# Performance work log

Hardware: AMD Instinct MI355X
Metric: run time of the kernel (lower is better)

## Reference

```python
import jax, jax.numpy as jnp
import numpy as np

B, E, NV = 2, 400000, 50000
DE, DV, DC, DOUT = 64, 64, 32, 64
DIN = DE + 2 * DV + DC  # 224


def setup_inputs() -> dict:
    key = jax.random.key(0)
    ks = jax.random.split(key, 7)
    edata = jax.random.normal(ks[0], (B, E, DE), dtype=jnp.float32)
    vdata = jax.random.normal(ks[1], (B, NV, DV), dtype=jnp.float32)
    cdata = jax.random.normal(ks[2], (B, DC), dtype=jnp.float32)
    sender_ids = jax.random.randint(ks[3], (B, E), 0, NV, dtype=jnp.int64)
    receiver_ids = jax.random.randint(ks[4], (B, E), 0, NV, dtype=jnp.int64)
    W = jax.random.normal(ks[5], (DIN, DOUT), dtype=jnp.float32) * (1.0 / np.sqrt(DIN))
    b = jnp.zeros((DOUT,), dtype=jnp.float32)
    return {"edata": edata, "vdata": vdata, "cdata": cdata,
            "sender_ids": sender_ids, "receiver_ids": receiver_ids,
            "W": W, "b": b}


def reference(edata, vdata, cdata, sender_ids, receiver_ids, W, b):
    # gather sender/receiver vertex features: [B,E,DV]
    sender_data = jnp.take_along_axis(vdata, sender_ids[..., None], axis=1)
    receiver_data = jnp.take_along_axis(vdata, receiver_ids[..., None], axis=1)
    # broadcast context per edge: [B,E,DC]
    curr_cdata = jnp.broadcast_to(cdata[:, None, :], (cdata.shape[0], edata.shape[1], cdata.shape[1]))
    # concat along feature dim -> [B,E,DIN], then per-edge-type MLP updater
    etin = jnp.concatenate((edata, sender_data, receiver_data, curr_cdata), axis=2)
    etout = jax.nn.relu(jnp.einsum("bei,io->beo", etin, W) + b)
    return etout
```

## Files before the change

### kernel.cpp

```cpp
#include <hip/hip_runtime.h>
#include <hip/hip_bf16.h>

typedef __bf16 bf16x8 __attribute__((ext_vector_type(8)));
typedef float  f32x4  __attribute__((ext_vector_type(4)));

#define DE_   64
#define DV_   64
#define DC_   32
#define DOUT_ 64
#define DIN_  224
#define NFRAG 28

__global__ void prep_w_kernel(const float* __restrict__ W, __bf16* __restrict__ wf) {
    int f    = blockIdx.x;
    int lane = threadIdx.x;
    int ks = f >> 2, nt = f & 3;
    int col = nt * 16 + (lane & 15);
    int k0  = ks * 32 + (lane >> 4) * 8;
    bf16x8 v;
#pragma unroll
    for (int j = 0; j < 8; ++j)
        v[j] = (__bf16)W[(k0 + j) * DOUT_ + col];
    reinterpret_cast<bf16x8*>(wf)[f * 64 + lane] = v;
}

__global__ __launch_bounds__(256, 6)
void edge_mlp_kernel(const float* __restrict__ edata,
                     const float* __restrict__ vdata,
                     const float* __restrict__ cdata,
                     const int*   __restrict__ snd,
                     const int*   __restrict__ rcv,
                     const __bf16* __restrict__ wf,
                     const float* __restrict__ bias,
                     float* __restrict__ out,
                     int NV, int n_tiles, int tiles_per_batch) {
    const int lane = threadIdx.x & 63;
    const int tile = blockIdx.x * (blockDim.x >> 6) + (threadIdx.x >> 6);
    if (tile >= n_tiles) return;

    const int lr = lane & 15;
    const int lg = lane >> 4;
    const int kl = lg * 8;

    const int  b   = (tile >= tiles_per_batch) ? 1 : 0;
    const long row = (long)tile * 16 + lr;
    const int  s   = snd[row];
    const int  r   = rcv[row];
    const float* vb = vdata + (long)b * NV * DV_;

    float4 f0[7], f1[7];
#pragma unroll
    for (int ks = 0; ks < 7; ++ks) {
        const float* p;
        if      (ks < 2) p = edata + row * DE_ + ks * 32 + kl;
        else if (ks < 4) p = vb + (long)s * DV_ + (ks - 2) * 32 + kl;
        else if (ks < 6) p = vb + (long)r * DV_ + (ks - 4) * 32 + kl;
        else             p = cdata + b * DC_ + kl;
        f0[ks] = *reinterpret_cast<const float4*>(p);
        f1[ks] = *reinterpret_cast<const float4*>(p + 4);
    }

    float bias_v[4];
#pragma unroll
    for (int nt = 0; nt < 4; ++nt) bias_v[nt] = bias[nt * 16 + lr];

    f32x4 acc[4];
#pragma unroll
    for (int nt = 0; nt < 4; ++nt) acc[nt] = f32x4{0.f, 0.f, 0.f, 0.f};

#pragma unroll
    for (int ks = 0; ks < 7; ++ks) {
        bf16x8 a;
        a[0] = (__bf16)f0[ks].x; a[1] = (__bf16)f0[ks].y;
        a[2] = (__bf16)f0[ks].z; a[3] = (__bf16)f0[ks].w;
        a[4] = (__bf16)f1[ks].x; a[5] = (__bf16)f1[ks].y;
        a[6] = (__bf16)f1[ks].z; a[7] = (__bf16)f1[ks].w;
#pragma unroll
        for (int nt = 0; nt < 4; ++nt) {
            bf16x8 w = reinterpret_cast<const bf16x8*>(wf)[(ks * 4 + nt) * 64 + lane];
            acc[nt] = __builtin_amdgcn_mfma_f32_16x16x32_bf16(a, w, acc[nt], 0, 0, 0);
        }
    }

    const long rb = (long)tile * 16;
#pragma unroll
    for (int nt = 0; nt < 4; ++nt) {
#pragma unroll
        for (int j = 0; j < 4; ++j) {
            float v = acc[nt][j] + bias_v[nt];
            v = v > 0.f ? v : 0.f;
            __builtin_nontemporal_store(v, &out[(rb + lg * 4 + j) * DOUT_ + nt * 16 + lr]);
        }
    }
}

extern "C" void kernel_launch(void* const* d_in, const int* in_sizes, int n_in,
                              void* d_out, int out_size, void* d_ws, size_t ws_size,
                              hipStream_t stream) {
    const float* edata = (const float*)d_in[0];
    const float* vdata = (const float*)d_in[1];
    const float* cdata = (const float*)d_in[2];
    const int*   snd   = (const int*)d_in[3];
    const int*   rcv   = (const int*)d_in[4];
    const float* W     = (const float*)d_in[5];
    const float* bias  = (const float*)d_in[6];
    float* out = (float*)d_out;

    const int Etot = in_sizes[3];
    const int Bb   = in_sizes[2] / DC_;
    const int E    = Etot / Bb;
    const int NV   = in_sizes[1] / (Bb * DV_);
    const int n_tiles = (Etot + 15) / 16;
    const int tiles_per_batch = E / 16;

    __bf16* wf = (__bf16*)d_ws;

    hipLaunchKernelGGL(prep_w_kernel, dim3(NFRAG), dim3(64), 0, stream, W, wf);

    const int waves_per_block = 4;
    const int blocks = (n_tiles + waves_per_block - 1) / waves_per_block;
    hipLaunchKernelGGL(edge_mlp_kernel, dim3(blocks), dim3(256), 0, stream,
                       edata, vdata, cdata, snd, rcv, wf, bias, out,
                       NV, n_tiles, tiles_per_batch);
}
```

Before: 135.1 us.

## Stage bf16 weight fragments in LDS and reorder gather loads

```diff
diff --git a/kernel.cpp b/kernel.cpp
--- a/kernel.cpp
+++ b/kernel.cpp
@@ -24,7 +24,7 @@
     reinterpret_cast<bf16x8*>(wf)[f * 64 + lane] = v;
 }
 
-__global__ __launch_bounds__(256, 6)
+__global__ __launch_bounds__(256, 4)
 void edge_mlp_kernel(const float* __restrict__ edata,
                      const float* __restrict__ vdata,
                      const float* __restrict__ cdata,
@@ -34,35 +34,55 @@
                      const float* __restrict__ bias,
                      float* __restrict__ out,
                      int NV, int n_tiles, int tiles_per_batch) {
-    const int lane = threadIdx.x & 63;
-    const int tile = blockIdx.x * (blockDim.x >> 6) + (threadIdx.x >> 6);
-    if (tile >= n_tiles) return;
+    __shared__ bf16x8 wlds[NFRAG * 64];
+
+    const int tid  = threadIdx.x;
+    const int lane = tid & 63;
+    const int tile = blockIdx.x * (blockDim.x >> 6) + (tid >> 6);
+    const bool active = tile < n_tiles;
 
     const int lr = lane & 15;
     const int lg = lane >> 4;
     const int kl = lg * 8;
 
     const int  b   = (tile >= tiles_per_batch) ? 1 : 0;
-    const long row = (long)tile * 16 + lr;
-    const int  s   = snd[row];
-    const int  r   = rcv[row];
-    const float* vb = vdata + (long)b * NV * DV_;
+    const long row = active ? ((long)tile * 16 + lr) : 0;
+
+    const int s = snd[row];
+    const int r = rcv[row];
 
     float4 f0[7], f1[7];
 #pragma unroll
-    for (int ks = 0; ks < 7; ++ks) {
-        const float* p;
-        if      (ks < 2) p = edata + row * DE_ + ks * 32 + kl;
-        else if (ks < 4) p = vb + (long)s * DV_ + (ks - 2) * 32 + kl;
-        else if (ks < 6) p = vb + (long)r * DV_ + (ks - 4) * 32 + kl;
-        else             p = cdata + b * DC_ + kl;
+    for (int ks = 0; ks < 2; ++ks) {
+        const float* p = edata + row * DE_ + ks * 32 + kl;
         f0[ks] = *reinterpret_cast<const float4*>(p);
         f1[ks] = *reinterpret_cast<const float4*>(p + 4);
     }
-
+    {
+        const float* p = cdata + b * DC_ + kl;
+        f0[6] = *reinterpret_cast<const float4*>(p);
+        f1[6] = *reinterpret_cast<const float4*>(p + 4);
+    }
     float bias_v[4];
 #pragma unroll
     for (int nt = 0; nt < 4; ++nt) bias_v[nt] = bias[nt * 16 + lr];
+
+    {
+        const bf16x8* wsrc = reinterpret_cast<const bf16x8*>(wf);
+#pragma unroll
+        for (int i = 0; i < 7; ++i)
+            wlds[i * 256 + tid] = wsrc[i * 256 + tid];
+    }
+    __syncthreads();
+
+    const float* vb = vdata + (long)b * NV * DV_;
+#pragma unroll
+    for (int ks = 2; ks < 6; ++ks) {
+        const float* p = (ks < 4) ? (vb + (long)s * DV_ + (ks - 2) * 32 + kl)
+                                  : (vb + (long)r * DV_ + (ks - 4) * 32 + kl);
+        f0[ks] = *reinterpret_cast<const float4*>(p);
+        f1[ks] = *reinterpret_cast<const float4*>(p + 4);
+    }
 
     f32x4 acc[4];
 #pragma unroll
@@ -77,10 +97,12 @@
         a[6] = (__bf16)f1[ks].z; a[7] = (__bf16)f1[ks].w;
 #pragma unroll
         for (int nt = 0; nt < 4; ++nt) {
-            bf16x8 w = reinterpret_cast<const bf16x8*>(wf)[(ks * 4 + nt) * 64 + lane];
+            bf16x8 w = wlds[(ks * 4 + nt) * 64 + lane];
             acc[nt] = __builtin_amdgcn_mfma_f32_16x16x32_bf16(a, w, acc[nt], 0, 0, 0);
         }
     }
+
+    if (!active) return;
 
     const long rb = (long)tile * 16;
 #pragma unroll
@@ -88,8 +110,7 @@
 #pragma unroll
         for (int j = 0; j < 4; ++j) {
             float v = acc[nt][j] + bias_v[nt];
-            v = v > 0.f ? v : 0.f;
-            __builtin_nontemporal_store(v, &out[(rb + lg * 4 + j) * DOUT_ + nt * 16 + lr]);
+            out[(rb + lg * 4 + j) * DOUT_ + nt * 16 + lr] = v > 0.f ? v : 0.f;
         }
     }
 }
```

Measured after the change: 136.3 us. No clear change (+0.9%).
